# Kernel optimization log

Hardware: AMD Instinct MI355X
Metric: run time of the kernel (lower is better)

Reference implementation:

```python
import jax, jax.numpy as jnp
import numpy as np

NUM_SELECTS = 2
NOISE_EPS = 0.01
LOSS_COEF = 0.01
INV_SQRT2 = 0.7071067811865476


def _phi(z):
    # standard normal CDF
    return 0.5 * (1.0 + jax.lax.erf(z * INV_SQRT2))


def _cv_squared(v, eps=1e-10):
    # torch .var() uses unbiased estimator (ddof=1)
    return jnp.var(v, ddof=1) / (jnp.mean(v) ** 2 + eps)


def setup_inputs() -> dict:
    key = jax.random.key(0)
    ks = jax.random.split(key, 5)
    T, D, E = 8192, 4096, 16
    return {
        "x": jax.random.normal(ks[0], (T, D), jnp.float32),
        "gate_w1": jax.random.normal(ks[1], (E, D), jnp.float32) * 0.02,
        "gate_w2": jax.random.normal(ks[2], (E, E), jnp.float32) * 0.02,
        "noise_w": jax.random.normal(ks[3], (E, D), jnp.float32) * 0.02,
        "noise": jax.random.normal(ks[4], (T, E), jnp.float32),
    }


def reference(x, gate_w1, gate_w2, noise_w, noise):
    T = x.shape[0]
    # gate network: Linear -> tanh -> Linear (no biases)
    logits_gate = jnp.tanh(x @ gate_w1.T) @ gate_w2.T          # [T, E]
    noise_control = jax.nn.softplus(x @ noise_w.T) + NOISE_EPS  # [T, E]
    logits_noise = noise * noise_control                        # [T, E]
    logits = logits_gate + logits_noise

    # top (k+1) for load-balancing thresholds
    top_logits, top_indices = jax.lax.top_k(logits, NUM_SELECTS + 1)
    top_k_logits = top_logits[:, :NUM_SELECTS]
    top_k_indices = top_indices[:, :NUM_SELECTS]
    top_k_scores = jax.nn.softmax(top_k_logits, axis=1)

    # importance: scatter top-k scores back to [T, E]
    rows = jnp.arange(T)[:, None]
    scores_filtered = jnp.zeros_like(logits).at[rows, top_k_indices].set(top_k_scores)
    importance = scores_filtered.sum(0)  # [E]

    # load: prob each expert would be in the top-k under the noise model
    thr_in = top_logits[:, NUM_SELECTS][:, None]        # (k+1)-th largest
    thr_out = top_logits[:, NUM_SELECTS - 1][:, None]   # k-th largest
    is_in = logits_noise > thr_in
    prob_if_in = _phi((logits_gate - thr_in) / noise_control)
    prob_if_out = _phi((logits_gate - thr_out) / noise_control)
    load = jnp.where(is_in, prob_if_in, prob_if_out).sum(0)  # [E]

    gate_loss = (_cv_squared(importance) + _cv_squared(load)) * LOSS_COEF
    return top_k_indices, top_k_scores, gate_loss
```

## Files before the change

kernel.cpp:

```cpp
#include <hip/hip_runtime.h>
#include <math.h>

#define TT 8192
#define DD 4096

typedef float  f32x4  __attribute__((ext_vector_type(4)));
typedef short  bf16x8 __attribute__((ext_vector_type(8)));
typedef unsigned int u32;

typedef __attribute__((address_space(3))) void        lds_vp;
typedef const __attribute__((address_space(1))) void  gbl_vp;
#define GLD(gp_, lp_) __builtin_amdgcn_global_load_lds((gbl_vp*)(gp_), (lds_vp*)(lp_), 16, 0, 0)

__global__ __launch_bounds__(128)
void split_w(const float* __restrict__ gw1, const float* __restrict__ nw,
             u32* __restrict__ wfrag) {
  const int s = blockIdx.x;
  const int t = threadIdx.x;
  const int h = t >> 6, l = t & 63;
  const int e = h * 16 + (l & 15);
  const float* src = ((e < 16) ? (gw1 + (size_t)e * DD) : (nw + (size_t)(e - 16) * DD))
                     + s * 32 + ((l >> 4) << 3);
  float f[8];
  *(float4*)&f[0] = *(const float4*)src;
  *(float4*)&f[4] = *(const float4*)(src + 4);
  u32 u0[8], u1[8], u2[8];
#pragma unroll
  for (int i = 0; i < 8; ++i) {
    u0[i] = __float_as_uint(f[i]);
    const float r1 = f[i] - __uint_as_float(u0[i] & 0xFFFF0000u);
    u1[i] = __float_as_uint(r1);
    const float r2 = r1 - __uint_as_float(u1[i] & 0xFFFF0000u);
    u2[i] = __float_as_uint(r2);
  }
  const size_t base = ((size_t)s * 2 + h) * 256 + l * 4;
#define PK(U) make_uint4((U[0]>>16)|(U[1]&0xFFFF0000u), (U[2]>>16)|(U[3]&0xFFFF0000u), \
                         (U[4]>>16)|(U[5]&0xFFFF0000u), (U[6]>>16)|(U[7]&0xFFFF0000u))
  *(uint4*)(wfrag + base)                 = PK(u0);
  *(uint4*)(wfrag + base + 128 * 512)     = PK(u1);
  *(uint4*)(wfrag + base + 2 * 128 * 512) = PK(u2);
#undef PK
}

__global__ __launch_bounds__(512, 4)
void gate_mega(const float* __restrict__ x, const u32* __restrict__ wfrag,
               const float* __restrict__ noise, const float* __restrict__ gw2,
               float* __restrict__ out, float* __restrict__ part2) {
  __shared__ __align__(16) float lds_x[8][3][512];
  __shared__ float red[8][512];
  __shared__ float sg2[256];
  const int t = threadIdx.x;
  const int w = t >> 6, l = t & 63;
  const int rt = blockIdx.x;
  if (t < 256) sg2[t] = gw2[t];

  const int r = l & 15, c = l >> 4;
  const float* gx = x + (size_t)(rt * 16 + r) * DD + w * 512 + (c << 3);
  const u32* wfl = wfrag + (size_t)l * 4 + (size_t)(w * 16) * 512;

  f32x4 ag0 = {0,0,0,0}, ag1 = ag0, ag2 = ag0, an0 = ag0, an1 = ag0, an2 = ag0;

  GLD(gx + 0 * 32,     &lds_x[w][0][0]);
  GLD(gx + 0 * 32 + 4, &lds_x[w][0][256]);
  GLD(gx + 1 * 32,     &lds_x[w][1][0]);
  GLD(gx + 1 * 32 + 4, &lds_x[w][1][256]);
  GLD(gx + 2 * 32,     &lds_x[w][2][0]);
  GLD(gx + 2 * 32 + 4, &lds_x[w][2][256]);

#pragma unroll
  for (int sl = 0; sl < 16; ++sl) {
    if (sl <= 13)      asm volatile("s_waitcnt vmcnt(4)" ::: "memory");
    else if (sl == 14) asm volatile("s_waitcnt vmcnt(2)" ::: "memory");
    else               asm volatile("s_waitcnt vmcnt(0)" ::: "memory");

    const float* xb = &lds_x[w][sl % 3][0];
    const f32x4 q0 = *(const f32x4*)(xb + (l << 2));
    const f32x4 q1 = *(const f32x4*)(xb + 256 + (l << 2));

    const u32* wb = wfl + (size_t)sl * 512;
    const bf16x8 bg0 = *(const bf16x8*)(wb);
    const bf16x8 bn0 = *(const bf16x8*)(wb + 256);
    const bf16x8 bg1 = *(const bf16x8*)(wb + 128 * 512);
    const bf16x8 bn1 = *(const bf16x8*)(wb + 128 * 512 + 256);
    const bf16x8 bg2 = *(const bf16x8*)(wb + 2 * 128 * 512);
    const bf16x8 bn2 = *(const bf16x8*)(wb + 2 * 128 * 512 + 256);

    u32 pk[12] __attribute__((aligned(16)));
#pragma unroll
    for (int p = 0; p < 4; ++p) {
      const float fa = (p < 2 ? q0 : q1)[(p & 1) * 2];
      const float fb = (p < 2 ? q0 : q1)[(p & 1) * 2 + 1];
      const u32  a  = __float_as_uint(fa);
      const float ra1 = fa - __uint_as_float(a & 0xFFFF0000u);
      const u32  a1 = __float_as_uint(ra1);
      const float ra2 = ra1 - __uint_as_float(a1 & 0xFFFF0000u);
      const u32  a2 = __float_as_uint(ra2);
      const u32  b  = __float_as_uint(fb);
      const float rb1 = fb - __uint_as_float(b & 0xFFFF0000u);
      const u32  b1 = __float_as_uint(rb1);
      const float rb2 = rb1 - __uint_as_float(b1 & 0xFFFF0000u);
      const u32  b2 = __float_as_uint(rb2);
      pk[p]     = (a  >> 16) | (b  & 0xFFFF0000u);
      pk[4 + p] = (a1 >> 16) | (b1 & 0xFFFF0000u);
      pk[8 + p] = (a2 >> 16) | (b2 & 0xFFFF0000u);
    }
    const bf16x8 a0 = *(const bf16x8*)&pk[0];
    const bf16x8 a1 = *(const bf16x8*)&pk[4];
    const bf16x8 a2 = *(const bf16x8*)&pk[8];

    asm volatile("s_waitcnt lgkmcnt(0)" ::: "memory");
    if (sl + 3 < 16) {
      GLD(gx + (sl + 3) * 32,     &lds_x[w][sl % 3][0]);
      GLD(gx + (sl + 3) * 32 + 4, &lds_x[w][sl % 3][256]);
    }

    ag0 = __builtin_amdgcn_mfma_f32_16x16x32_bf16(a0, bg0, ag0, 0, 0, 0);
    an0 = __builtin_amdgcn_mfma_f32_16x16x32_bf16(a0, bn0, an0, 0, 0, 0);
    ag1 = __builtin_amdgcn_mfma_f32_16x16x32_bf16(a0, bg1, ag1, 0, 0, 0);
    an1 = __builtin_amdgcn_mfma_f32_16x16x32_bf16(a0, bn1, an1, 0, 0, 0);
    ag2 = __builtin_amdgcn_mfma_f32_16x16x32_bf16(a1, bg0, ag2, 0, 0, 0);
    an2 = __builtin_amdgcn_mfma_f32_16x16x32_bf16(a1, bn0, an2, 0, 0, 0);
    ag0 = __builtin_amdgcn_mfma_f32_16x16x32_bf16(a0, bg2, ag0, 0, 0, 0);
    an0 = __builtin_amdgcn_mfma_f32_16x16x32_bf16(a0, bn2, an0, 0, 0, 0);
    ag1 = __builtin_amdgcn_mfma_f32_16x16x32_bf16(a1, bg1, ag1, 0, 0, 0);
    an1 = __builtin_amdgcn_mfma_f32_16x16x32_bf16(a1, bn1, an1, 0, 0, 0);
    ag2 = __builtin_amdgcn_mfma_f32_16x16x32_bf16(a2, bg0, ag2, 0, 0, 0);
    an2 = __builtin_amdgcn_mfma_f32_16x16x32_bf16(a2, bn0, an2, 0, 0, 0);
  }

  const f32x4 cg = ag0 + ag1 + ag2;
  const f32x4 cn = an0 + an1 + an2;
#pragma unroll
  for (int j = 0; j < 4; ++j) {
    red[w][r * 16 + (c * 4 + j)]        = cg[j];
    red[w][(16 + r) * 16 + (c * 4 + j)] = cn[j];
  }
  __syncthreads();
  {
    float s = red[0][t];
#pragma unroll
    for (int ww = 1; ww < 8; ++ww) s += red[ww][t];
    red[0][t] = s;
  }
  __syncthreads();

  if (t < 16) {
    const int row = rt * 16 + t;
    float dot[32];
#pragma unroll
    for (int e = 0; e < 32; ++e) dot[e] = red[0][e * 16 + t];
    float h[16];
#pragma unroll
    for (int e = 0; e < 16; ++e) h[e] = tanhf(dot[e]);
    float lg[16], nc[16], ln[16], lo[16];
#pragma unroll
    for (int j = 0; j < 16; ++j) {
      float s = 0.f;
#pragma unroll
      for (int e = 0; e < 16; ++e) s = fmaf(h[e], sg2[j * 16 + e], s);
      lg[j] = s;
      const float v = dot[16 + j];
      nc[j] = fmaxf(v, 0.f) + log1pf(expf(-fabsf(v))) + 0.01f;
      ln[j] = noise[(size_t)row * 16 + j] * nc[j];
      lo[j] = lg[j] + ln[j];
    }
    int i0 = 0; float m0 = lo[0];
#pragma unroll
    for (int j = 1; j < 16; ++j) if (lo[j] > m0) { m0 = lo[j]; i0 = j; }
    int i1 = -1; float m1 = -1e30f;
#pragma unroll
    for (int j = 0; j < 16; ++j) if (j != i0 && lo[j] > m1) { m1 = lo[j]; i1 = j; }
    float m2 = -1e30f;
#pragma unroll
    for (int j = 0; j < 16; ++j) if (j != i0 && j != i1 && lo[j] > m2) m2 = lo[j];

    const float e1 = expf(m1 - m0);
    const float s0 = 1.f / (1.f + e1);
    const float s1 = e1 / (1.f + e1);
    out[(size_t)row * 2]             = (float)i0;
    out[(size_t)row * 2 + 1]         = (float)i1;
    out[16384 + (size_t)row * 2]     = s0;
    out[16384 + (size_t)row * 2 + 1] = s1;

    float cacc[32];
#pragma unroll
    for (int j = 0; j < 16; ++j) {
      cacc[j] = (j == i0) ? s0 : ((j == i1) ? s1 : 0.f);
      const bool in = ln[j] > m2;
      const float thr = in ? m2 : m1;
      const float z = (lg[j] - thr) / nc[j];
      cacc[16 + j] = 0.5f * (1.f + erff(z * 0.70710678118654752f));
    }
#pragma unroll
    for (int off = 1; off < 16; off <<= 1) {
#pragma unroll
      for (int k = 0; k < 32; ++k) cacc[k] += __shfl_xor(cacc[k], off, 16);
    }
    float v0 = 0.f, v1 = 0.f;
#pragma unroll
    for (int k = 0; k < 16; ++k) if (t == k) { v0 = cacc[k]; v1 = cacc[16 + k]; }
    part2[(size_t)rt * 32 + t]      = v0;
    part2[(size_t)rt * 32 + 16 + t] = v1;
  }
}

__global__ __launch_bounds__(256)
void gate_loss_k(const float* __restrict__ part2, float* __restrict__ out) {
  __shared__ float sred[8][32];
  const int t = threadIdx.x;
  const int k = t & 31, s = t >> 5;
  float acc = 0.f;
#pragma unroll 8
  for (int i = 0; i < 64; ++i) acc += part2[(size_t)(s * 64 + i) * 32 + k];
  sred[s][k] = acc;
  __syncthreads();
  if (t == 0) {
    float res = 0.f;
    for (int g = 0; g < 2; ++g) {
      float vals[16];
      float mu = 0.f;
      for (int j = 0; j < 16; ++j) {
        float s2 = 0.f;
        for (int ss = 0; ss < 8; ++ss) s2 += sred[ss][g * 16 + j];
        vals[j] = s2;
        mu += s2;
      }
      mu *= (1.f / 16.f);
      float var = 0.f;
      for (int j = 0; j < 16; ++j) { const float d = vals[j] - mu; var += d * d; }
      var *= (1.f / 15.f);
      res += var / (mu * mu + 1e-10f);
    }
    out[32768] = res * 0.01f;
  }
}

extern "C" void kernel_launch(void* const* d_in, const int* in_sizes, int n_in,
                              void* d_out, int out_size, void* d_ws, size_t ws_size,
                              hipStream_t stream) {
  const float* x     = (const float*)d_in[0];
  const float* gw1   = (const float*)d_in[1];
  const float* gw2   = (const float*)d_in[2];
  const float* nw    = (const float*)d_in[3];
  const float* noise = (const float*)d_in[4];
  float* out   = (float*)d_out;
  u32*   wfrag = (u32*)d_ws;
  float* part2 = (float*)((char*)d_ws + (size_t)768 * 1024);
  split_w<<<128, 128, 0, stream>>>(gw1, nw, wfrag);
  gate_mega<<<512, 512, 0, stream>>>(x, wfrag, noise, gw2, out, part2);
  gate_loss_k<<<1, 256, 0, stream>>>(part2, out);
}
```

Before: 63.07 us.

## Restage x loads into larger double-buffered batches with row-contiguous coalescing

```diff
diff --git a/kernel.cpp b/kernel.cpp
--- a/kernel.cpp
+++ b/kernel.cpp
@@ -42,11 +42,11 @@
 #undef PK
 }
 
-__global__ __launch_bounds__(512, 4)
+__global__ __launch_bounds__(512, 2)
 void gate_mega(const float* __restrict__ x, const u32* __restrict__ wfrag,
                const float* __restrict__ noise, const float* __restrict__ gw2,
                float* __restrict__ out, float* __restrict__ part2) {
-  __shared__ __align__(16) float lds_x[8][3][512];
+  __shared__ __align__(16) float ldsx[8][2][2048];
   __shared__ float red[8][512];
   __shared__ float sg2[256];
   const int t = threadIdx.x;
@@ -55,78 +55,81 @@
   if (t < 256) sg2[t] = gw2[t];
 
   const int r = l & 15, c = l >> 4;
-  const float* gx = x + (size_t)(rt * 16 + r) * DD + w * 512 + (c << 3);
   const u32* wfl = wfrag + (size_t)l * 4 + (size_t)(w * 16) * 512;
+  const float* gxb = x + (size_t)(rt * 16 + (l >> 5)) * DD + w * 512 + ((l & 31) << 2);
+
+#define ISSUE_BATCH(b_) \
+  { _Pragma("unroll") for (int i = 0; i < 8; ++i) \
+      GLD(gxb + (size_t)(2 * i) * DD + (b_) * 128, &ldsx[w][(b_) & 1][i * 256]); }
+
+  ISSUE_BATCH(0)
+  ISSUE_BATCH(1)
 
   f32x4 ag0 = {0,0,0,0}, ag1 = ag0, ag2 = ag0, an0 = ag0, an1 = ag0, an2 = ag0;
 
-  GLD(gx + 0 * 32,     &lds_x[w][0][0]);
-  GLD(gx + 0 * 32 + 4, &lds_x[w][0][256]);
-  GLD(gx + 1 * 32,     &lds_x[w][1][0]);
-  GLD(gx + 1 * 32 + 4, &lds_x[w][1][256]);
-  GLD(gx + 2 * 32,     &lds_x[w][2][0]);
-  GLD(gx + 2 * 32 + 4, &lds_x[w][2][256]);
-
-#pragma unroll
-  for (int sl = 0; sl < 16; ++sl) {
-    if (sl <= 13)      asm volatile("s_waitcnt vmcnt(4)" ::: "memory");
-    else if (sl == 14) asm volatile("s_waitcnt vmcnt(2)" ::: "memory");
-    else               asm volatile("s_waitcnt vmcnt(0)" ::: "memory");
-
-    const float* xb = &lds_x[w][sl % 3][0];
-    const f32x4 q0 = *(const f32x4*)(xb + (l << 2));
-    const f32x4 q1 = *(const f32x4*)(xb + 256 + (l << 2));
-
-    const u32* wb = wfl + (size_t)sl * 512;
-    const bf16x8 bg0 = *(const bf16x8*)(wb);
-    const bf16x8 bn0 = *(const bf16x8*)(wb + 256);
-    const bf16x8 bg1 = *(const bf16x8*)(wb + 128 * 512);
-    const bf16x8 bn1 = *(const bf16x8*)(wb + 128 * 512 + 256);
-    const bf16x8 bg2 = *(const bf16x8*)(wb + 2 * 128 * 512);
-    const bf16x8 bn2 = *(const bf16x8*)(wb + 2 * 128 * 512 + 256);
-
-    u32 pk[12] __attribute__((aligned(16)));
-#pragma unroll
-    for (int p = 0; p < 4; ++p) {
-      const float fa = (p < 2 ? q0 : q1)[(p & 1) * 2];
-      const float fb = (p < 2 ? q0 : q1)[(p & 1) * 2 + 1];
-      const u32  a  = __float_as_uint(fa);
-      const float ra1 = fa - __uint_as_float(a & 0xFFFF0000u);
-      const u32  a1 = __float_as_uint(ra1);
-      const float ra2 = ra1 - __uint_as_float(a1 & 0xFFFF0000u);
-      const u32  a2 = __float_as_uint(ra2);
-      const u32  b  = __float_as_uint(fb);
-      const float rb1 = fb - __uint_as_float(b & 0xFFFF0000u);
-      const u32  b1 = __float_as_uint(rb1);
-      const float rb2 = rb1 - __uint_as_float(b1 & 0xFFFF0000u);
-      const u32  b2 = __float_as_uint(rb2);
-      pk[p]     = (a  >> 16) | (b  & 0xFFFF0000u);
-      pk[4 + p] = (a1 >> 16) | (b1 & 0xFFFF0000u);
-      pk[8 + p] = (a2 >> 16) | (b2 & 0xFFFF0000u);
-    }
-    const bf16x8 a0 = *(const bf16x8*)&pk[0];
-    const bf16x8 a1 = *(const bf16x8*)&pk[4];
-    const bf16x8 a2 = *(const bf16x8*)&pk[8];
-
-    asm volatile("s_waitcnt lgkmcnt(0)" ::: "memory");
-    if (sl + 3 < 16) {
-      GLD(gx + (sl + 3) * 32,     &lds_x[w][sl % 3][0]);
-      GLD(gx + (sl + 3) * 32 + 4, &lds_x[w][sl % 3][256]);
-    }
-
-    ag0 = __builtin_amdgcn_mfma_f32_16x16x32_bf16(a0, bg0, ag0, 0, 0, 0);
-    an0 = __builtin_amdgcn_mfma_f32_16x16x32_bf16(a0, bn0, an0, 0, 0, 0);
-    ag1 = __builtin_amdgcn_mfma_f32_16x16x32_bf16(a0, bg1, ag1, 0, 0, 0);
-    an1 = __builtin_amdgcn_mfma_f32_16x16x32_bf16(a0, bn1, an1, 0, 0, 0);
-    ag2 = __builtin_amdgcn_mfma_f32_16x16x32_bf16(a1, bg0, ag2, 0, 0, 0);
-    an2 = __builtin_amdgcn_mfma_f32_16x16x32_bf16(a1, bn0, an2, 0, 0, 0);
-    ag0 = __builtin_amdgcn_mfma_f32_16x16x32_bf16(a0, bg2, ag0, 0, 0, 0);
-    an0 = __builtin_amdgcn_mfma_f32_16x16x32_bf16(a0, bn2, an0, 0, 0, 0);
-    ag1 = __builtin_amdgcn_mfma_f32_16x16x32_bf16(a1, bg1, ag1, 0, 0, 0);
-    an1 = __builtin_amdgcn_mfma_f32_16x16x32_bf16(a1, bn1, an1, 0, 0, 0);
-    ag2 = __builtin_amdgcn_mfma_f32_16x16x32_bf16(a2, bg0, ag2, 0, 0, 0);
-    an2 = __builtin_amdgcn_mfma_f32_16x16x32_bf16(a2, bn0, an2, 0, 0, 0);
-  }
+#pragma unroll
+  for (int b = 0; b < 4; ++b) {
+    if (b < 3) asm volatile("s_waitcnt vmcnt(8)" ::: "memory");
+    else       asm volatile("s_waitcnt vmcnt(0)" ::: "memory");
+
+#pragma unroll
+    for (int j = 0; j < 4; ++j) {
+      const int sl = b * 4 + j;
+      const float* xb = &ldsx[w][b & 1][(r >> 1) * 256 + (r & 1) * 128 + j * 32 + (c << 3)];
+      const f32x4 q0 = *(const f32x4*)(xb);
+      const f32x4 q1 = *(const f32x4*)(xb + 4);
+
+      const u32* wb = wfl + (size_t)sl * 512;
+      const bf16x8 bg0 = *(const bf16x8*)(wb);
+      const bf16x8 bn0 = *(const bf16x8*)(wb + 256);
+      const bf16x8 bg1 = *(const bf16x8*)(wb + 128 * 512);
+      const bf16x8 bn1 = *(const bf16x8*)(wb + 128 * 512 + 256);
+      const bf16x8 bg2 = *(const bf16x8*)(wb + 2 * 128 * 512);
+      const bf16x8 bn2 = *(const bf16x8*)(wb + 2 * 128 * 512 + 256);
+
+      u32 pk[12] __attribute__((aligned(16)));
+#pragma unroll
+      for (int p = 0; p < 4; ++p) {
+        const float fa = (p < 2 ? q0 : q1)[(p & 1) * 2];
+        const float fb = (p < 2 ? q0 : q1)[(p & 1) * 2 + 1];
+        const u32  a  = __float_as_uint(fa);
+        const float ra1 = fa - __uint_as_float(a & 0xFFFF0000u);
+        const u32  a1 = __float_as_uint(ra1);
+        const float ra2 = ra1 - __uint_as_float(a1 & 0xFFFF0000u);
+        const u32  a2 = __float_as_uint(ra2);
+        const u32  b_  = __float_as_uint(fb);
+        const float rb1 = fb - __uint_as_float(b_ & 0xFFFF0000u);
+        const u32  b1 = __float_as_uint(rb1);
+        const float rb2 = rb1 - __uint_as_float(b1 & 0xFFFF0000u);
+        const u32  b2 = __float_as_uint(rb2);
+        pk[p]     = (a  >> 16) | (b_  & 0xFFFF0000u);
+        pk[4 + p] = (a1 >> 16) | (b1 & 0xFFFF0000u);
+        pk[8 + p] = (a2 >> 16) | (b2 & 0xFFFF0000u);
+      }
+      const bf16x8 a0 = *(const bf16x8*)&pk[0];
+      const bf16x8 a1 = *(const bf16x8*)&pk[4];
+      const bf16x8 a2 = *(const bf16x8*)&pk[8];
+
+      ag0 = __builtin_amdgcn_mfma_f32_16x16x32_bf16(a0, bg0, ag0, 0, 0, 0);
+      an0 = __builtin_amdgcn_mfma_f32_16x16x32_bf16(a0, bn0, an0, 0, 0, 0);
+      ag1 = __builtin_amdgcn_mfma_f32_16x16x32_bf16(a0, bg1, ag1, 0, 0, 0);
+      an1 = __builtin_amdgcn_mfma_f32_16x16x32_bf16(a0, bn1, an1, 0, 0, 0);
+      ag2 = __builtin_amdgcn_mfma_f32_16x16x32_bf16(a1, bg0, ag2, 0, 0, 0);
+      an2 = __builtin_amdgcn_mfma_f32_16x16x32_bf16(a1, bn0, an2, 0, 0, 0);
+      ag0 = __builtin_amdgcn_mfma_f32_16x16x32_bf16(a0, bg2, ag0, 0, 0, 0);
+      an0 = __builtin_amdgcn_mfma_f32_16x16x32_bf16(a0, bn2, an0, 0, 0, 0);
+      ag1 = __builtin_amdgcn_mfma_f32_16x16x32_bf16(a1, bg1, ag1, 0, 0, 0);
+      an1 = __builtin_amdgcn_mfma_f32_16x16x32_bf16(a1, bn1, an1, 0, 0, 0);
+      ag2 = __builtin_amdgcn_mfma_f32_16x16x32_bf16(a2, bg0, ag2, 0, 0, 0);
+      an2 = __builtin_amdgcn_mfma_f32_16x16x32_bf16(a2, bn0, an2, 0, 0, 0);
+    }
+
+    if (b + 2 < 4) {
+      asm volatile("s_waitcnt lgkmcnt(0)" ::: "memory");
+      ISSUE_BATCH(b + 2)
+    }
+  }
+#undef ISSUE_BATCH
 
   const f32x4 cg = ag0 + ag1 + ag2;
   const f32x4 cn = an0 + an1 + an2;
```

Measured after the change: 71.12 us. +12.8%, slower.
